# Kernel tuning notes

Hardware: AMD Instinct MI355X
Metric: run time of the kernel (lower is better)

## Reference

```python
import jax, jax.numpy as jnp
import numpy as np

D_MODEL = 1024
B, S = 4, 2048


def setup_inputs() -> dict:
    key = jax.random.key(0)
    kx, km, kq, kk, kv, ko = jax.random.split(key, 6)
    x = jax.random.normal(kx, (B, S, D_MODEL), dtype=jnp.float32)
    mask = jax.random.randint(km, (B, S, S), 0, 2).astype(jnp.bool_)
    # flax Dense default kernel init: lecun_normal-ish; plain scaled normal is fine for a reference
    init_scale = 1.0 / np.sqrt(D_MODEL)
    Wq = jax.random.normal(kq, (D_MODEL, D_MODEL), dtype=jnp.float32) * init_scale
    Wk = jax.random.normal(kk, (D_MODEL, D_MODEL), dtype=jnp.float32) * init_scale
    Wv = jax.random.normal(kv, (D_MODEL, D_MODEL), dtype=jnp.float32) * init_scale
    Wo = jax.random.normal(ko, (D_MODEL, D_MODEL), dtype=jnp.float32) * init_scale
    return {"x": x, "mask": mask, "Wq": Wq, "Wk": Wk, "Wv": Wv, "Wo": Wo}


def reference(x, mask, Wq, Wk, Wv, Wo):
    # QKV projections (use_bias=False)
    q = jnp.einsum('bsd,de->bse', x, Wq)
    k = jnp.einsum('bsd,de->bse', x, Wk)
    v = jnp.einsum('bsd,de->bse', x, Wv)
    scale = jnp.sqrt(jnp.asarray(q.shape[-1], x.dtype)).astype(x.dtype)
    # [B, S, S] attention scores
    attn_scores = jnp.einsum('bqd,bkd->bqk', q, k) / scale
    attn_scores = jnp.where(mask, attn_scores, jnp.asarray(-1e10, x.dtype))
    attn_weights = jax.nn.softmax(attn_scores, axis=-1)
    attn_output = jnp.einsum('bqk,bkd->bqd', attn_weights, v)
    return jnp.einsum('bsd,de->bse', attn_output, Wo)
```

## Files before the change

kernel.cpp:

```cpp
#include <hip/hip_runtime.h>


#define DM 1024
#define SQ 2048
#define NB 4
typedef unsigned short U16;
typedef short bhalf8 __attribute__((ext_vector_type(8)));
typedef float f32x4 __attribute__((ext_vector_type(4)));

__device__ inline U16 f2bf(float f) {
  unsigned int u = __float_as_uint(f);
  u += 0x7FFFu + ((u >> 16) & 1u);
  return (U16)(u >> 16);
}
__device__ inline float2 bfp2(unsigned int u) {
  float2 r;
  r.x = __uint_as_float(u << 16);
  r.y = __uint_as_float(u & 0xffff0000u);
  return r;
}
__device__ inline unsigned int packbf(float a, float b) {
  return (unsigned int)f2bf(a) | ((unsigned int)f2bf(b) << 16);
}

__device__ __forceinline__ void gload16(const U16* g, const U16* l) {
  unsigned int m0v =
      (unsigned int)__builtin_amdgcn_readfirstlane((int)(unsigned long long)l);
  asm volatile("s_mov_b32 m0, %0\n\t"
               "global_load_lds_dwordx4 %1, off"
               :
               : "s"(m0v), "v"(g)
               : "memory");
}

__global__ __launch_bounds__(256) void conv_f32_bf16(
    const float* __restrict__ src, U16* __restrict__ dst, float* __restrict__ rs) {
  int idx = blockIdx.x * 256 + threadIdx.x;
  if (idx < NB * SQ) rs[idx] = 0.f;
  int i = idx * 8;
  float4 a = *(const float4*)(src + i);
  float4 b = *(const float4*)(src + i + 4);
  uint4 w;
  w.x = packbf(a.x, a.y); w.y = packbf(a.z, a.w);
  w.z = packbf(b.x, b.y); w.w = packbf(b.z, b.w);
  *(uint4*)(dst + i) = w;
}

__device__ inline void ldcvt16(const float* p, U16* d) {
#pragma unroll
  for (int i = 0; i < 4; ++i) {
    float4 f = *(const float4*)(p + i * 4);
    d[i * 4 + 0] = f2bf(f.x); d[i * 4 + 1] = f2bf(f.y);
    d[i * 4 + 2] = f2bf(f.z); d[i * 4 + 3] = f2bf(f.w);
  }
}
__device__ inline void ldcvt16(const U16* p, U16* d) {
  uint4 a = *(const uint4*)p;
  uint4 b = *(const uint4*)(p + 8);
  *(uint4*)d = a;
  *(uint4*)(d + 8) = b;
}

__global__ __launch_bounds__(256) void transp_w4(
    const float* __restrict__ Wq, const float* __restrict__ Wk,
    const float* __restrict__ Wo, const float* __restrict__ Wv,
    U16* __restrict__ WT, U16* __restrict__ WoT, U16* __restrict__ Wv16) {
  __shared__ U16 tile[64][72];
  const int z = blockIdx.z;
  const int r0 = blockIdx.y * 64, c0 = blockIdx.x * 64;
  const int t = threadIdx.x;
  const int tr = t >> 2, tc = (t & 3) * 16;
  if (z == 3) {
    U16 vals[16];
    ldcvt16(Wv + (size_t)(r0 + tr) * DM + c0 + tc, vals);
    U16* op = Wv16 + (size_t)(r0 + tr) * DM + c0 + tc;
    *(uint4*)op = *(uint4*)&vals[0];
    *(uint4*)(op + 8) = *(uint4*)&vals[8];
    return;
  }
  const float* src = (z == 0) ? Wq : (z == 1) ? Wk : Wo;
  U16* d = (z == 2) ? WoT : WT + (size_t)z * DM * DM;
  ldcvt16(src + (size_t)(r0 + tr) * DM + c0 + tc, &tile[tr][tc]);
  __syncthreads();
  U16 vals[16];
#pragma unroll
  for (int m = 0; m < 16; ++m) vals[m] = tile[tc + m][tr];
  U16* op = d + (size_t)(c0 + tr) * DM + r0 + tc;
  *(uint4*)op = *(uint4*)&vals[0];
  *(uint4*)(op + 8) = *(uint4*)&vals[8];
}

__global__ __launch_bounds__(256) void transp_bf16(
    const U16* __restrict__ src, U16* __restrict__ dst, int R, int C) {
  __shared__ U16 tile[64][72];
  const int z = blockIdx.z;
  src += (size_t)z * R * C;
  dst += (size_t)z * R * C;
  const int r0 = blockIdx.y * 64, c0 = blockIdx.x * 64;
  const int t = threadIdx.x;
  const int tr = t >> 2, tc = (t & 3) * 16;
  ldcvt16(src + (size_t)(r0 + tr) * C + c0 + tc, &tile[tr][tc]);
  __syncthreads();
  U16 vals[16];
#pragma unroll
  for (int m = 0; m < 16; ++m) vals[m] = tile[tc + m][tr];
  U16* op = dst + (size_t)(c0 + tr) * R + r0 + tc;
  *(uint4*)op = *(uint4*)&vals[0];
  *(uint4*)(op + 8) = *(uint4*)&vals[8];
}

template <int EP>
__global__ __launch_bounds__(256) void gemm_mfma(
    const U16* __restrict__ A, const U16* __restrict__ B, void* __restrict__ Cv,
    int M, int N, int K, long long sA, long long sB, long long sC,
    const int* __restrict__ mask, float* __restrict__ rowsum, float scale) {
  __shared__ U16 As[128 * 72];
  __shared__ U16 Bs[128 * 72];
  const int t = threadIdx.x;
  const int lane = t & 63, wave = t >> 6;
  const int wm = wave >> 1, wn = wave & 1;
  const int q = lane >> 4, ln = lane & 15;
  const int z = blockIdx.z;
  const int m0 = blockIdx.y * 128, n0 = blockIdx.x * 128;
  A += (size_t)z * sA;
  B += (size_t)z * sB;

  f32x4 acc[4][4] = {};

  const int srow = t >> 3;
  const int scol = (t & 7) * 8;

  for (int k0 = 0; k0 < K; k0 += 64) {
    const U16* ga = A + (size_t)(m0 + srow) * K + k0 + scol;
    const U16* gb = B + (size_t)(n0 + srow) * K + k0 + scol;
#pragma unroll
    for (int it = 0; it < 4; ++it) {
      uint4 va = *(const uint4*)(ga + (size_t)it * 32 * K);
      uint4 vb = *(const uint4*)(gb + (size_t)it * 32 * K);
      *(uint4*)&As[(it * 32 + srow) * 72 + scol] = va;
      *(uint4*)&Bs[(it * 32 + srow) * 72 + scol] = vb;
    }
    __syncthreads();
#pragma unroll
    for (int kk = 0; kk < 64; kk += 32) {
      bhalf8 af[4], bg[4];
#pragma unroll
      for (int i = 0; i < 4; ++i) {
        af[i] = *(const bhalf8*)&As[(wm * 64 + i * 16 + ln) * 72 + kk + q * 8];
        bg[i] = *(const bhalf8*)&Bs[(wn * 64 + i * 16 + ln) * 72 + kk + q * 8];
      }
#pragma unroll
      for (int i = 0; i < 4; ++i)
#pragma unroll
        for (int j = 0; j < 4; ++j)
          acc[i][j] = __builtin_amdgcn_mfma_f32_16x16x32_bf16(af[i], bg[j], acc[i][j], 0, 0, 0);
    }
    __syncthreads();
  }

#pragma unroll
  for (int i = 0; i < 4; ++i) {
#pragma unroll
    for (int r = 0; r < 4; ++r) {
      const int rr = m0 + wm * 64 + i * 16 + q * 4 + r;
      float linv = 0.f;
      if constexpr (EP == 2) linv = 1.0f / (rowsum[(size_t)z * M + rr] + 1e-30f);
      float psum = 0.f;
#pragma unroll
      for (int j = 0; j < 4; ++j) {
        const int c = n0 + wn * 64 + j * 16 + ln;
        float v = acc[i][j][r];
        if constexpr (EP == 0) {
          ((U16*)Cv)[(size_t)z * sC + (size_t)rr * N + c] = f2bf(v);
        } else if constexpr (EP == 1) {
          int mk = mask[((size_t)z * M + rr) * N + c];
          float p = mk ? __expf(v * scale) : 0.f;
          U16 pb = f2bf(p);
          ((U16*)Cv)[(size_t)z * sC + (size_t)rr * N + c] = pb;
          psum += __uint_as_float((unsigned int)pb << 16);
        } else {
          ((float*)Cv)[(size_t)z * sC + (size_t)rr * N + c] = v * linv;
        }
      }
      if constexpr (EP == 1) {
#pragma unroll
        for (int off = 8; off > 0; off >>= 1) psum += __shfl_xor(psum, off, 64);
        if (ln == 0) atomicAdd(&rowsum[(size_t)z * M + rr], psum);
      }
    }
  }
}

template <int EP, int FM>
__global__ __launch_bounds__(512) void gemm2(
    const U16* __restrict__ A, const U16* __restrict__ B, void* __restrict__ Cv,
    int M, int N, int K, long long sA, long long sB, long long sC,
    const int* __restrict__ mask, float* __restrict__ rowsum, float scale) {
  constexpr int WN = (FM == 4) ? 2 : 4;
  constexpr int BN = WN * 64;
  __shared__ __attribute__((aligned(16))) U16 As[2][256 * 64];
  __shared__ __attribute__((aligned(16))) U16 Bs[2][BN * 64];
  const int t = threadIdx.x;
  const int lane = t & 63, wave = t >> 6;
  const int wm = wave / WN, wn = wave % WN;
  const int q = lane >> 4, ln = lane & 15;
  const int z = blockIdx.z;
  const int m0 = blockIdx.y * 256, n0 = blockIdx.x * BN;
  const U16* Ab = A + (size_t)z * sA + (size_t)m0 * K;
  const U16* Bb = B + (size_t)z * sB + (size_t)n0 * K;
  const U16* gA = Ab + (size_t)(wave * 8 + (lane >> 3)) * K + (lane & 7) * 8;
  const U16* gB = Bb + (size_t)(wave * 8 + (lane >> 3)) * K + (lane & 7) * 8;
  const U16* lA = &As[0][wave * 8 * 64];
  const U16* lB = &Bs[0][wave * 8 * 64];

  f32x4 acc[FM][4] = {};
  const int NT = K >> 6;

#define STAGE2(bufi, koff)                                                   \
  {                                                                          \
    _Pragma("unroll") for (int c = 0; c < 4; ++c)                            \
        gload16(gA + (size_t)(c * 64) * K + (koff),                          \
                lA + (bufi) * (256 * 64) + c * (64 * 64));                   \
    _Pragma("unroll") for (int c = 0; c < BN / 64; ++c)                      \
        gload16(gB + (size_t)(c * 64) * K + (koff),                          \
                lB + (bufi) * (BN * 64) + c * (64 * 64));                    \
  }

#define COMPUTE2(bufi)                                                       \
  {                                                                          \
    _Pragma("unroll") for (int kk = 0; kk < 64; kk += 32) {                  \
      bhalf8 af[FM], bg[4];                                                  \
      _Pragma("unroll") for (int i = 0; i < FM; ++i)                         \
          af[i] = *(const bhalf8*)&As[bufi][(wm * (FM * 16) + i * 16 + ln) * 64 + kk + q * 8]; \
      _Pragma("unroll") for (int j = 0; j < 4; ++j)                          \
          bg[j] = *(const bhalf8*)&Bs[bufi][(wn * 64 + j * 16 + ln) * 64 + kk + q * 8]; \
      _Pragma("unroll") for (int i = 0; i < FM; ++i)                         \
          _Pragma("unroll") for (int j = 0; j < 4; ++j)                      \
              acc[i][j] = __builtin_amdgcn_mfma_f32_16x16x32_bf16(af[i], bg[j], acc[i][j], 0, 0, 0); \
    }                                                                        \
  }

#define VMBAR                                            \
  {                                                      \
    asm volatile("s_waitcnt vmcnt(0)" ::: "memory");     \
    __syncthreads();                                     \
  }

  STAGE2(0, 0);
  VMBAR;
  for (int tk = 2; tk < NT; tk += 2) {
    STAGE2(1, (tk - 1) * 64);
    COMPUTE2(0);
    VMBAR;
    STAGE2(0, tk * 64);
    COMPUTE2(1);
    VMBAR;
  }
  STAGE2(1, (NT - 1) * 64);
  COMPUTE2(0);
  VMBAR;
  COMPUTE2(1);
#undef STAGE2
#undef COMPUTE2
#undef VMBAR

#pragma unroll
  for (int i = 0; i < FM; ++i) {
#pragma unroll
    for (int r = 0; r < 4; ++r) {
      const int rr = m0 + wm * (FM * 16) + i * 16 + q * 4 + r;
      float linv = 0.f;
      if constexpr (EP == 2) linv = 1.0f / (rowsum[(size_t)z * M + rr] + 1e-30f);
      float psum = 0.f;
#pragma unroll
      for (int j = 0; j < 4; ++j) {
        const int c = n0 + wn * 64 + j * 16 + ln;
        float v = acc[i][j][r];
        if constexpr (EP == 0) {
          ((U16*)Cv)[(size_t)z * sC + (size_t)rr * N + c] = f2bf(v);
        } else if constexpr (EP == 1) {
          int mk = mask[((size_t)z * M + rr) * N + c];
          float p = mk ? __expf(v * scale) : 0.f;
          U16 pb = f2bf(p);
          ((U16*)Cv)[(size_t)z * sC + (size_t)rr * N + c] = pb;
          psum += __uint_as_float((unsigned int)pb << 16);
        } else {
          ((float*)Cv)[(size_t)z * sC + (size_t)rr * N + c] = v * linv;
        }
      }
      if constexpr (EP == 1) {
#pragma unroll
        for (int off = 8; off > 0; off >>= 1) psum += __shfl_xor(psum, off, 64);
        if (ln == 0) atomicAdd(&rowsum[(size_t)z * M + rr], psum);
      }
    }
  }
}

__device__ inline float4 load4(const float* p) { return *(const float4*)p; }
__device__ inline float4 load4(const U16* p) {
  uint2 w = *(const uint2*)p;
  float2 f0 = bfp2(w.x), f1 = bfp2(w.y);
  return make_float4(f0.x, f0.y, f1.x, f1.y);
}
__device__ inline void store4(float* p, float a, float b, float c, float d) {
  *(float4*)p = make_float4(a, b, c, d);
}
__device__ inline void store4(U16* p, float a, float b, float c, float d) {
  uint2 w;
  w.x = packbf(a, b);
  w.y = packbf(c, d);
  *(uint2*)p = w;
}
template <typename TA, typename TB, typename TC>
__global__ __launch_bounds__(256) void gemm_t(
    const TA* __restrict__ A, const TB* __restrict__ B,
    TC* __restrict__ C, int M, int N, int K) {
  __shared__ float As[16][64];
  __shared__ float Bs[16][64];
  const int t = threadIdx.x;
  const int tx = t & 15, ty = t >> 4;
  const int m0 = blockIdx.y * 64;
  const int n0 = blockIdx.x * 64;
  const int arow = t >> 2, akq = (t & 3) * 4;
  const int brow = t >> 4, bcg = (t & 15) * 4;
  float acc[4][4] = {};
  for (int k0 = 0; k0 < K; k0 += 16) {
    {
      float4 f = load4(A + (size_t)(m0 + arow) * K + k0 + akq);
      As[akq + 0][arow] = f.x; As[akq + 1][arow] = f.y;
      As[akq + 2][arow] = f.z; As[akq + 3][arow] = f.w;
    }
    {
      float4 f = load4(B + (size_t)(k0 + brow) * N + n0 + bcg);
      *(float4*)&Bs[brow][bcg] = f;
    }
    __syncthreads();
#pragma unroll
    for (int kk = 0; kk < 16; ++kk) {
      float4 a = *(const float4*)&As[kk][ty * 4];
      float4 b = *(const float4*)&Bs[kk][tx * 4];
      float av[4] = {a.x, a.y, a.z, a.w};
      float bv[4] = {b.x, b.y, b.z, b.w};
#pragma unroll
      for (int i = 0; i < 4; ++i)
#pragma unroll
        for (int j = 0; j < 4; ++j) acc[i][j] += av[i] * bv[j];
    }
    __syncthreads();
  }
#pragma unroll
  for (int i = 0; i < 4; ++i)
    store4(&C[(size_t)(m0 + ty * 4 + i) * N + n0 + tx * 4],
           acc[i][0], acc[i][1], acc[i][2], acc[i][3]);
}
__global__ __launch_bounds__(256) void flash_wave(
    const U16* __restrict__ Q, const U16* __restrict__ Kd,
    const U16* __restrict__ V, const int* __restrict__ mask,
    U16* __restrict__ O) {
  __shared__ float q_s[4][DM];
  const int t = threadIdx.x;
  const int w = t >> 6;
  const int lane = t & 63;
  const int row = blockIdx.x * 4 + w;
  const int b = row >> 11;
  const size_t bo = (size_t)b * SQ * DM;
  const size_t mrow0 = (size_t)row * SQ;
  {
    const U16* qp = Q + (size_t)row * DM + lane * 16;
    uint4 w0 = *(const uint4*)qp;
    uint4 w1 = *(const uint4*)(qp + 8);
    float* dst = &q_s[w][lane * 16];
    float2 f;
    f = bfp2(w0.x); dst[0] = f.x;  dst[1] = f.y;
    f = bfp2(w0.y); dst[2] = f.x;  dst[3] = f.y;
    f = bfp2(w0.z); dst[4] = f.x;  dst[5] = f.y;
    f = bfp2(w0.w); dst[6] = f.x;  dst[7] = f.y;
    f = bfp2(w1.x); dst[8] = f.x;  dst[9] = f.y;
    f = bfp2(w1.y); dst[10] = f.x; dst[11] = f.y;
    f = bfp2(w1.z); dst[12] = f.x; dst[13] = f.y;
    f = bfp2(w1.w); dst[14] = f.x; dst[15] = f.y;
  }
  __syncthreads();
  float m = -3.0e38f, l = 0.f;
  float o[16] = {};
  const int dbase = lane * 16;
  const float* qrow = q_s[w];
  for (int j0 = 0; j0 < SQ; j0 += 64) {
    float s;
    {
      const U16* kp = Kd + bo + (size_t)(j0 + lane) * DM;
      float acc = 0.f;
      for (int d = 0; d < DM; d += 8) {
        uint4 kw = *(const uint4*)(kp + d);
        float2 a0 = bfp2(kw.x), a1 = bfp2(kw.y), a2 = bfp2(kw.z), a3 = bfp2(kw.w);
        acc += qrow[d] * a0.x + qrow[d + 1] * a0.y + qrow[d + 2] * a1.x +
               qrow[d + 3] * a1.y + qrow[d + 4] * a2.x + qrow[d + 5] * a2.y +
               qrow[d + 6] * a3.x + qrow[d + 7] * a3.y;
      }
      s = acc * 0.03125f;
      if (mask[mrow0 + j0 + lane] == 0) s = -1e10f;
    }
    float ms = s;
#pragma unroll
    for (int off = 32; off > 0; off >>= 1) ms = fmaxf(ms, __shfl_xor(ms, off, 64));
    float mn = fmaxf(m, ms);
    float alpha = __expf(m - mn);
    float p = __expf(s - mn);
    float ps = p;
#pragma unroll
    for (int off = 32; off > 0; off >>= 1) ps += __shfl_xor(ps, off, 64);
    l = l * alpha + ps;
    m = mn;
#pragma unroll
    for (int k = 0; k < 16; ++k) o[k] *= alpha;
    const U16* vp = V + bo + (size_t)j0 * DM + dbase;
    for (int j = 0; j < 64; ++j) {
      float pj = __shfl(p, j, 64);
      uint4 v0 = *(const uint4*)(vp + (size_t)j * DM);
      uint4 v1 = *(const uint4*)(vp + (size_t)j * DM + 8);
      float2 f0 = bfp2(v0.x), f1 = bfp2(v0.y), f2 = bfp2(v0.z), f3 = bfp2(v0.w);
      float2 g0 = bfp2(v1.x), g1 = bfp2(v1.y), g2 = bfp2(v1.z), g3 = bfp2(v1.w);
      o[0] += pj * f0.x;  o[1] += pj * f0.y;  o[2] += pj * f1.x;  o[3] += pj * f1.y;
      o[4] += pj * f2.x;  o[5] += pj * f2.y;  o[6] += pj * f3.x;  o[7] += pj * f3.y;
      o[8] += pj * g0.x;  o[9] += pj * g0.y;  o[10] += pj * g1.x; o[11] += pj * g1.y;
      o[12] += pj * g2.x; o[13] += pj * g2.y; o[14] += pj * g3.x; o[15] += pj * g3.y;
    }
  }
  float linv = (l > 0.f) ? (1.0f / l) : 0.f;
  U16* op = O + (size_t)row * DM + dbase;
  uint4 r0, r1;
  r0.x = packbf(o[0] * linv, o[1] * linv);
  r0.y = packbf(o[2] * linv, o[3] * linv);
  r0.z = packbf(o[4] * linv, o[5] * linv);
  r0.w = packbf(o[6] * linv, o[7] * linv);
  r1.x = packbf(o[8] * linv, o[9] * linv);
  r1.y = packbf(o[10] * linv, o[11] * linv);
  r1.z = packbf(o[12] * linv, o[13] * linv);
  r1.w = packbf(o[14] * linv, o[15] * linv);
  *(uint4*)op = r0;
  *(uint4*)(op + 8) = r1;
}

extern "C" void kernel_launch(void* const* d_in, const int* in_sizes, int n_in,
                              void* d_out, int out_size, void* d_ws, size_t ws_size,
                              hipStream_t stream) {
  const float* x  = (const float*)d_in[0];
  const int* mask = (const int*)d_in[1];
  const float* Wq = (const float*)d_in[2];
  const float* Wk = (const float*)d_in[3];
  const float* Wv = (const float*)d_in[4];
  const float* Wo = (const float*)d_in[5];
  float* out = (float*)d_out;

  const size_t MB = 1u << 20;
  const size_t E = (size_t)NB * SQ * DM;
  const size_t WE = (size_t)DM * DM;

  if (ws_size >= 121 * MB) {
    char* ws = (char*)d_ws;
    U16* WT   = (U16*)ws;
    U16* WoT  = (U16*)(ws + 6 * MB);
    U16* x16  = (U16*)(ws + 8 * MB);
    U16* Q16  = (U16*)(ws + 24 * MB);
    U16* K16  = (U16*)(ws + 40 * MB);
    U16* U16b = (U16*)(ws + 56 * MB);
    U16* Wv16 = (U16*)(ws + 72 * MB);
    U16* UT16 = (U16*)(ws + 72 * MB);
    U16* P16  = (U16*)(ws + 88 * MB);
    float* rs = (float*)(ws + 120 * MB);

    conv_f32_bf16<<<dim3(E / (256 * 8)), 256, 0, stream>>>(x, x16, rs);
    transp_w4<<<dim3(16, 16, 4), 256, 0, stream>>>(Wq, Wk, Wo, Wv, WT, WoT, Wv16);

    gemm_mfma<0><<<dim3(DM / 128, DM / 128, 1), 256, 0, stream>>>(
        WoT, Wv16, WT + 2 * WE, DM, DM, DM, 0, 0, 0, nullptr, nullptr, 0.f);

    gemm2<0, 4><<<dim3(DM / 128, (NB * SQ) / 256, 3), 512, 0, stream>>>(
        x16, WT, Q16, NB * SQ, DM, DM,
        0, (long long)WE, (long long)E, nullptr, nullptr, 0.f);

    transp_bf16<<<dim3(DM / 64, SQ / 64, NB), 256, 0, stream>>>(U16b, UT16, SQ, DM);

    gemm2<1, 8><<<dim3(SQ / 256, SQ / 256, NB), 512, 0, stream>>>(
        Q16, K16, P16, SQ, SQ, DM,
        (long long)SQ * DM, (long long)SQ * DM, (long long)SQ * SQ,
        mask, rs, 0.03125f);

    gemm2<2, 4><<<dim3(DM / 128, SQ / 256, NB), 512, 0, stream>>>(
        P16, UT16, out, SQ, DM, SQ,
        (long long)SQ * SQ, (long long)DM * SQ, (long long)SQ * DM,
        nullptr, rs, 0.f);
  } else {
    U16* Kw = (U16*)d_ws;
    U16* Vw = Kw + E;
    U16* Qw = Vw + E;
    U16* Ow = Qw;
    dim3 blk(256);
    dim3 gg(DM / 64, (NB * SQ) / 64);
    gemm_t<float, float, U16><<<gg, blk, 0, stream>>>(x, Wk, Kw, NB * SQ, DM, DM);
    gemm_t<float, float, U16><<<gg, blk, 0, stream>>>(x, Wv, Vw, NB * SQ, DM, DM);
    gemm_t<float, float, U16><<<gg, blk, 0, stream>>>(x, Wq, Qw, NB * SQ, DM, DM);
    flash_wave<<<dim3((NB * SQ) / 4), blk, 0, stream>>>(Qw, Kw, Vw, mask, Ow);
    gemm_t<U16, float, float><<<gg, blk, 0, stream>>>(Ow, Wo, out, NB * SQ, DM, DM);
  }
}
```

Baseline: 348.1 us.

## Rewrite bf16 GEMM mainloop with XOR-swizzled LDS and quarter-tile interleaved pipeline

Replaces the double-buffered GEMM kernel with an 8-wave variant that splits each K-tile into four sub-quadrants. Global loads for the next tile are interleaved with MFMA blocks, using partial vmcnt waits, raw barriers and s_setprio around MFMA. LDS columns are XOR-swizzled to avoid bank conflicts, and rows are remapped so each half-tile is contiguous. The aim is to hide memory latency and LDS conflicts behind compute, at the cost of more barriers and complex index math that is easy to get wrong.

```diff
diff --git a/kernel.cpp b/kernel.cpp
--- a/kernel.cpp
+++ b/kernel.cpp
@@ -191,84 +191,140 @@
   }
 }
 
-template <int EP, int FM>
-__global__ __launch_bounds__(512) void gemm2(
+template <int EP, int WM>
+__global__ __launch_bounds__(512, 1) void gemm8(
     const U16* __restrict__ A, const U16* __restrict__ B, void* __restrict__ Cv,
     int M, int N, int K, long long sA, long long sB, long long sC,
     const int* __restrict__ mask, float* __restrict__ rowsum, float scale) {
-  constexpr int WN = (FM == 4) ? 2 : 4;
+  constexpr int WN = 8 / WM;
   constexpr int BN = WN * 64;
-  __shared__ __attribute__((aligned(16))) U16 As[2][256 * 64];
-  __shared__ __attribute__((aligned(16))) U16 Bs[2][BN * 64];
+  constexpr int MR = 256 / WM;
+  constexpr int FM = MR / 16;
+  constexpr int IMq = FM / 2;
+  constexpr int HB = BN / 2;
+  constexpr int CB = HB / 64;
+  constexpr int VW = 4 + 2 * CB;
+  __shared__ __attribute__((aligned(16))) U16 Abuf[2][256 * 64];
+  __shared__ __attribute__((aligned(16))) U16 Bbuf[2][BN * 64];
   const int t = threadIdx.x;
   const int lane = t & 63, wave = t >> 6;
   const int wm = wave / WN, wn = wave % WN;
   const int q = lane >> 4, ln = lane & 15;
+  const int lxor = ln & 7;
   const int z = blockIdx.z;
   const int m0 = blockIdx.y * 256, n0 = blockIdx.x * BN;
-  const U16* Ab = A + (size_t)z * sA + (size_t)m0 * K;
-  const U16* Bb = B + (size_t)z * sB + (size_t)n0 * K;
-  const U16* gA = Ab + (size_t)(wave * 8 + (lane >> 3)) * K + (lane & 7) * 8;
-  const U16* gB = Bb + (size_t)(wave * 8 + (lane >> 3)) * K + (lane & 7) * 8;
-  const U16* lA = &As[0][wave * 8 * 64];
-  const U16* lB = &Bs[0][wave * 8 * 64];
+  const U16* Abase = A + (size_t)z * sA + (size_t)m0 * K;
+  const U16* Bbase = B + (size_t)z * sB + (size_t)n0 * K;
+
+  const int pr = wave * 8 + (lane >> 3);
+  const int cchunk = (((lane & 7) ^ ((lane >> 3) & 7)) << 3);
+  int la[4];
+#pragma unroll
+  for (int c = 0; c < 4; ++c) {
+    int p = c * 64 + pr;
+    int mh = p >> 7, q64 = p & 127;
+    la[c] = (q64 / (MR / 2)) * MR + mh * (MR / 2) + (q64 % (MR / 2));
+  }
+  int lb[4] = {0, 0, 0, 0};
+#pragma unroll
+  for (int c = 0; c < 2 * CB; ++c) {
+    int p = c * 64 + pr;
+    int nh = p / HB, rem = p % HB;
+    lb[c] = (rem >> 5) * 64 + nh * 32 + (rem & 31);
+  }
+  const U16* gA0 = Abase + (size_t)la[0] * K + cchunk;
+  const U16* gA1 = Abase + (size_t)la[1] * K + cchunk;
+  const U16* gA2 = Abase + (size_t)la[2] * K + cchunk;
+  const U16* gA3 = Abase + (size_t)la[3] * K + cchunk;
+  const U16* gB0 = Bbase + (size_t)lb[0] * K + cchunk;
+  const U16* gB1 = (CB == 2) ? Bbase + (size_t)lb[1] * K + cchunk : gB0;
+  const U16* gB2 = Bbase + (size_t)lb[CB] * K + cchunk;
+  const U16* gB3 = (CB == 2) ? Bbase + (size_t)lb[3] * K + cchunk : gB2;
+  const int wofs = wave * 8 * 64;
+
+#define ST_AX(bi, ko) { gload16(gA0 + (ko), &Abuf[bi][0 * 64 + wofs]);         \
+                        gload16(gA1 + (ko), &Abuf[bi][64 * 64 + wofs]); }
+#define ST_AY(bi, ko) { gload16(gA2 + (ko), &Abuf[bi][128 * 64 + wofs]);       \
+                        gload16(gA3 + (ko), &Abuf[bi][192 * 64 + wofs]); }
+#define ST_BE(bi, ko) { gload16(gB0 + (ko), &Bbuf[bi][0 * 64 + wofs]);         \
+                        if (CB == 2) gload16(gB1 + (ko), &Bbuf[bi][64 * 64 + wofs]); }
+#define ST_BO(bi, ko) { gload16(gB2 + (ko), &Bbuf[bi][HB * 64 + wofs]);        \
+                        if (CB == 2) gload16(gB3 + (ko), &Bbuf[bi][(HB + 64) * 64 + wofs]); }
 
   f32x4 acc[FM][4] = {};
+  bhalf8 af[IMq][2], bgE[2][2], bgO[2][2];
+
+#define LDA(bi, mh) {                                                          \
+  _Pragma("unroll") for (int im = 0; im < IMq; ++im)                           \
+  _Pragma("unroll") for (int kx = 0; kx < 2; ++kx)                             \
+    af[im][kx] = *(const bhalf8*)&Abuf[bi][                                    \
+        ((mh) * 128 + wm * (MR / 2) + im * 16 + ln) * 64 +                     \
+        (((kx * 4 + q) ^ lxor) << 3)]; }
+#define LDB(bi, nh, BG) {                                                      \
+  _Pragma("unroll") for (int jn = 0; jn < 2; ++jn)                             \
+  _Pragma("unroll") for (int kx = 0; kx < 2; ++kx)                             \
+    BG[jn][kx] = *(const bhalf8*)&Bbuf[bi][                                    \
+        ((nh) * HB + wn * 32 + jn * 16 + ln) * 64 +                            \
+        (((kx * 4 + q) ^ lxor) << 3)]; }
+#define MQ(mh, nh, BG) {                                                       \
+  __builtin_amdgcn_s_setprio(1);                                               \
+  _Pragma("unroll") for (int im = 0; im < IMq; ++im)                           \
+  _Pragma("unroll") for (int jn = 0; jn < 2; ++jn)                             \
+  _Pragma("unroll") for (int kx = 0; kx < 2; ++kx)                             \
+    acc[(mh) * IMq + im][(nh) * 2 + jn] =                                      \
+        __builtin_amdgcn_mfma_f32_16x16x32_bf16(                               \
+            af[im][kx], BG[jn][kx], acc[(mh) * IMq + im][(nh) * 2 + jn],       \
+            0, 0, 0);                                                          \
+  __builtin_amdgcn_s_setprio(0); }
+#define WAITV(n) asm volatile("s_waitcnt vmcnt(%0)" :: "i"(n) : "memory")
+#define BAR() __builtin_amdgcn_s_barrier()
+#define LGKM0() asm volatile("s_waitcnt lgkmcnt(0)" ::: "memory")
+
+#define TILE8(bi, nbi, kA, kB)                                                 \
+  {                                                                            \
+    ST_BO(nbi, kA); WAITV(VW);                                                 \
+    LDA(bi, 0); LDB(bi, 0, bgE);                                               \
+    BAR(); LGKM0(); MQ(0, 0, bgE); BAR();                                      \
+    ST_AY(nbi, kA); WAITV(VW);                                                 \
+    LDB(bi, 1, bgO);                                                           \
+    BAR(); LGKM0(); MQ(0, 1, bgO); BAR();                                      \
+    ST_AX(bi, kB); WAITV(VW);                                                  \
+    LDA(bi, 1);                                                                \
+    BAR(); LGKM0(); MQ(1, 0, bgE); BAR();                                      \
+    ST_BE(bi, kB); WAITV(VW);                                                  \
+    BAR(); LGKM0(); MQ(1, 1, bgO); BAR();                                      \
+  }
+
   const int NT = K >> 6;
-
-#define STAGE2(bufi, koff)                                                   \
-  {                                                                          \
-    _Pragma("unroll") for (int c = 0; c < 4; ++c)                            \
-        gload16(gA + (size_t)(c * 64) * K + (koff),                          \
-                lA + (bufi) * (256 * 64) + c * (64 * 64));                   \
-    _Pragma("unroll") for (int c = 0; c < BN / 64; ++c)                      \
-        gload16(gB + (size_t)(c * 64) * K + (koff),                          \
-                lB + (bufi) * (BN * 64) + c * (64 * 64));                    \
-  }
-
-#define COMPUTE2(bufi)                                                       \
-  {                                                                          \
-    _Pragma("unroll") for (int kk = 0; kk < 64; kk += 32) {                  \
-      bhalf8 af[FM], bg[4];                                                  \
-      _Pragma("unroll") for (int i = 0; i < FM; ++i)                         \
-          af[i] = *(const bhalf8*)&As[bufi][(wm * (FM * 16) + i * 16 + ln) * 64 + kk + q * 8]; \
-      _Pragma("unroll") for (int j = 0; j < 4; ++j)                          \
-          bg[j] = *(const bhalf8*)&Bs[bufi][(wn * 64 + j * 16 + ln) * 64 + kk + q * 8]; \
-      _Pragma("unroll") for (int i = 0; i < FM; ++i)                         \
-          _Pragma("unroll") for (int j = 0; j < 4; ++j)                      \
-              acc[i][j] = __builtin_amdgcn_mfma_f32_16x16x32_bf16(af[i], bg[j], acc[i][j], 0, 0, 0); \
-    }                                                                        \
-  }
-
-#define VMBAR                                            \
-  {                                                      \
-    asm volatile("s_waitcnt vmcnt(0)" ::: "memory");     \
-    __syncthreads();                                     \
-  }
-
-  STAGE2(0, 0);
-  VMBAR;
-  for (int tk = 2; tk < NT; tk += 2) {
-    STAGE2(1, (tk - 1) * 64);
-    COMPUTE2(0);
-    VMBAR;
-    STAGE2(0, tk * 64);
-    COMPUTE2(1);
-    VMBAR;
-  }
-  STAGE2(1, (NT - 1) * 64);
-  COMPUTE2(0);
-  VMBAR;
-  COMPUTE2(1);
-#undef STAGE2
-#undef COMPUTE2
-#undef VMBAR
+  ST_AX(0, 0); ST_BE(0, 0); ST_BO(0, 0); ST_AY(0, 0);
+  ST_AX(1, 64); ST_BE(1, 64);
+  WAITV(VW); BAR();
+  for (int tt = 0; tt < NT; tt += 2) {
+    const int k1 = (tt + 1) * 64;
+    const int k2 = (tt + 2 < NT) ? (tt + 2) * 64 : 0;
+    const int k3 = (tt + 3 < NT) ? (tt + 3) * 64 : 0;
+    TILE8(0, 1, k1, k2);
+    TILE8(1, 0, k2, k3);
+  }
+  WAITV(0);
+
+#undef ST_AX
+#undef ST_AY
+#undef ST_BE
+#undef ST_BO
+#undef LDA
+#undef LDB
+#undef MQ
+#undef WAITV
+#undef BAR
+#undef LGKM0
+#undef TILE8
 
 #pragma unroll
   for (int i = 0; i < FM; ++i) {
 #pragma unroll
     for (int r = 0; r < 4; ++r) {
-      const int rr = m0 + wm * (FM * 16) + i * 16 + q * 4 + r;
+      const int rr = m0 + wm * MR + i * 16 + q * 4 + r;
       float linv = 0.f;
       if constexpr (EP == 2) linv = 1.0f / (rowsum[(size_t)z * M + rr] + 1e-30f);
       float psum = 0.f;
@@ -476,18 +532,18 @@
     gemm_mfma<0><<<dim3(DM / 128, DM / 128, 1), 256, 0, stream>>>(
         WoT, Wv16, WT + 2 * WE, DM, DM, DM, 0, 0, 0, nullptr, nullptr, 0.f);
 
-    gemm2<0, 4><<<dim3(DM / 128, (NB * SQ) / 256, 3), 512, 0, stream>>>(
+    gemm8<0, 4><<<dim3(DM / 128, (NB * SQ) / 256, 3), 512, 0, stream>>>(
         x16, WT, Q16, NB * SQ, DM, DM,
         0, (long long)WE, (long long)E, nullptr, nullptr, 0.f);
 
     transp_bf16<<<dim3(DM / 64, SQ / 64, NB), 256, 0, stream>>>(U16b, UT16, SQ, DM);
 
-    gemm2<1, 8><<<dim3(SQ / 256, SQ / 256, NB), 512, 0, stream>>>(
+    gemm8<1, 2><<<dim3(SQ / 256, SQ / 256, NB), 512, 0, stream>>>(
         Q16, K16, P16, SQ, SQ, DM,
         (long long)SQ * DM, (long long)SQ * DM, (long long)SQ * SQ,
         mask, rs, 0.03125f);
 
-    gemm2<2, 4><<<dim3(DM / 128, SQ / 256, NB), 512, 0, stream>>>(
+    gemm8<2, 4><<<dim3(DM / 128, SQ / 256, NB), 512, 0, stream>>>(
         P16, UT16, out, SQ, DM, SQ,
         (long long)SQ * SQ, (long long)DM * SQ, (long long)SQ * DM,
         nullptr, rs, 0.f);
```

New measurement: 339.6 us. 2.5% less time.
